# Optimization experiments

Hardware: AMD Instinct MI355X
Metric: run time of the kernel (lower is better)

Reference implementation:

```python
import jax, jax.numpy as jnp
import numpy as np

N_NODES = 50000
N_EDGES = 800000
ATOM_DIM = 128
BOND_DIM = 16
HID = 128
STEPS = 4


def setup_inputs() -> dict:
    key = jax.random.key(0)
    k1, k2, k3, k4, k5, k6 = jax.random.split(key, 6)
    atoms = jax.random.normal(k1, (N_NODES, ATOM_DIM), dtype=jnp.float32)
    bonds = jax.random.normal(k2, (N_NODES, BOND_DIM), dtype=jnp.float32)
    pairs = jax.random.randint(k3, (N_EDGES, 2), 0, N_NODES)
    # sort rows by target id (tf.math.segment_sum expects sorted segment ids)
    order = jnp.argsort(pairs[:, 0])
    pairs = pairs[order].astype(jnp.int64)
    # learned parameters (glorot-ish scaling)
    kernel = jax.random.normal(k4, (ATOM_DIM, BOND_DIM * BOND_DIM), dtype=jnp.float32) * (2.0 / (ATOM_DIM + BOND_DIM * BOND_DIM)) ** 0.5
    bias = jnp.zeros((BOND_DIM * BOND_DIM,), dtype=jnp.float32)
    weight_node = jax.random.normal(k5, (BOND_DIM, HID), dtype=jnp.float32) * (2.0 / (BOND_DIM + HID)) ** 0.5
    weight_node_inp = jax.random.normal(k6, (BOND_DIM, HID), dtype=jnp.float32) * (2.0 / (BOND_DIM + HID)) ** 0.5
    return {"atoms": atoms, "bonds": bonds, "pairs": pairs,
            "kernel": kernel, "bias": bias,
            "weight_node": weight_node, "weight_node_inp": weight_node_inp}


def reference(atoms, bonds, pairs, kernel, bias, weight_node, weight_node_inp):
    n, bd = bonds.shape
    # per-node transform -> [N, bd, bd] message matrices
    A = (atoms @ kernel + bias).reshape(n, bd, bd)
    src = pairs[:, 0]
    nbr = pairs[:, 1]
    # gather bonds of neighbors, apply source-node matrix per edge: [E, bd]
    trans = jnp.einsum('eij,ej->ei', A[src], bonds[nbr])
    # scatter-add back to nodes keyed on pairs[:,0]
    aggregate = jax.ops.segment_sum(trans, src, num_segments=n)  # [N, bd]
    # step loop: aggregate is never updated in the original, so each step
    # computes the identical result; compute once and replicate.
    nodes = aggregate @ weight_node            # [N, hid]
    edges = jax.nn.relu(bonds @ weight_node_inp)  # [N, hid]
    result = jax.nn.relu(nodes + edges)
    return jnp.stack([result] * STEPS)  # [steps, N, hid]
```

## Files before the change

### kernel.cpp

```cpp
#include <hip/hip_runtime.h>

typedef __attribute__((ext_vector_type(8))) short bf16x8;
typedef __attribute__((ext_vector_type(4))) float f32x4;

constexpr int N       = 50000;
constexpr int NE      = 800000;
constexpr int AD      = 128;
constexpr int BD      = 16;
constexpr int BD2     = 256;
constexpr int HIDDEN  = 128;
constexpr int NB      = 64;
constexpr int SSTR    = 20;
constexpr int OSTR    = 132;

__device__ inline short f2bf(float f) {
    union U { float f; unsigned u; } v; v.f = f;
    unsigned r = v.u + 0x7fffu + ((v.u >> 16) & 1u);
    return (short)(r >> 16);
}

__global__ __launch_bounds__(256) void prep_frags(
    const float* __restrict__ kmat,
    const float* __restrict__ Wn,
    const float* __restrict__ Wi,
    short* __restrict__ kbf,
    short* __restrict__ wbf)
{
    int t = blockIdx.x * 256 + threadIdx.x;
    if (t < 4096) {
        int u = t >> 6, l = t & 63;
        int nf = u >> 2, kk = u & 3;
        int col = nf * 16 + (l & 15);
        int k0  = kk * 32 + (l >> 4) * 8;
        bf16x8 o;
#pragma unroll
        for (int j = 0; j < 8; ++j) o[j] = f2bf(kmat[(size_t)(k0 + j) * BD2 + col]);
        *(bf16x8*)(kbf + (size_t)t * 8) = o;
    } else if (t < 4096 + 1024) {
        int t2 = t - 4096;
        int u = t2 >> 6, l = t2 & 63;
        int m = u >> 3, nf2 = u & 7;
        const float* W = m ? Wi : Wn;
        int col = nf2 * 16 + (l & 15);
        int k0  = (l >> 4) * 8;
        bf16x8 o;
#pragma unroll
        for (int j = 0; j < 8; ++j) {
            int k = k0 + j;
            o[j] = (k < 16) ? f2bf(W[(size_t)k * HIDDEN + col]) : (short)0;
        }
        *(bf16x8*)(wbf + (size_t)t2 * 8) = o;
    }
}

__global__ __launch_bounds__(256) void scatter_tile(
    const int*  __restrict__ pairs,
    const float* __restrict__ bonds,
    float* __restrict__ S)
{
    __shared__ float st[NB * SSTR];

    const int tid = threadIdx.x;
    const int nb  = blockIdx.x * NB;

    for (int i = tid; i < NB * SSTR; i += 256) st[i] = 0.f;

    int wlo = nb * 16 - 4096; if (wlo < 0) wlo = 0;
    int whi = (nb + NB) * 16 + 4096; if (whi > NE) whi = NE;
    if (wlo > 0  && pairs[2 * wlo] >= nb)      wlo = 0;
    if (whi < NE && pairs[2 * whi] <  nb + NB) whi = NE;
    int eLo, eHi;
    {
        int s = wlo, e = whi;
        while (s < e) { int m = (s + e) >> 1; if (pairs[2 * m] < nb) s = m + 1; else e = m; }
        eLo = s;
    }
    {
        int s = eLo, e = whi;
        while (s < e) { int m = (s + e) >> 1; if (pairs[2 * m] < nb + NB) s = m + 1; else e = m; }
        eHi = s;
    }
    __syncthreads();

    {
        const int g = tid >> 4;
        const int c = tid & 15;
        const int nE = eHi - eLo;
        const int cg = (nE + 15) >> 4;
        int gs = eLo + g * cg;
        int ge = gs + cg; if (ge > eHi) ge = eHi;
        int cur = -1; float acc = 0.f;
        int e = gs;
        for (; e + 4 <= ge; e += 4) {
            int2 pb[4]; float vb[4];
#pragma unroll
            for (int i = 0; i < 4; ++i) pb[i] = *(const int2*)(pairs + 2 * (e + i));
#pragma unroll
            for (int i = 0; i < 4; ++i) vb[i] = bonds[(size_t)pb[i].y * BD + c];
#pragma unroll
            for (int i = 0; i < 4; ++i) {
                if (pb[i].x != cur) {
                    if (cur >= 0) atomicAdd(&st[(cur - nb) * SSTR + c], acc);
                    acc = 0.f; cur = pb[i].x;
                }
                acc += vb[i];
            }
        }
        for (; e < ge; ++e) {
            int2 p = *(const int2*)(pairs + 2 * e);
            float v = bonds[(size_t)p.y * BD + c];
            if (p.x != cur) {
                if (cur >= 0) atomicAdd(&st[(cur - nb) * SSTR + c], acc);
                acc = 0.f; cur = p.x;
            }
            acc += v;
        }
        if (cur >= 0) atomicAdd(&st[(cur - nb) * SSTR + c], acc);
    }
    __syncthreads();

    {
        int node = tid >> 2;
        int c4   = (tid & 3) * 4;
        if (nb + node < N) {
            f32x4 v = *(const f32x4*)(&st[node * SSTR + c4]);
            *(f32x4*)(S + (size_t)(nb + node) * BD + c4) = v;
        }
    }
}

__global__ __launch_bounds__(256, 3) void gemm_contract(
    const float* __restrict__ atoms,
    const short* __restrict__ kbf,
    const float* __restrict__ bias,
    float* Sagg)
{
    __shared__ float ag[NB * SSTR];

    const int tid = threadIdx.x;
    const int w   = tid >> 6;
    const int l   = tid & 63;
    const int lq  = l >> 4;
    const int lj  = l & 15;
    const int nb  = blockIdx.x * NB;

    bf16x8 afrag[4][4];
    float4 sval[4];
#pragma unroll
    for (int ng = 0; ng < 4; ++ng) {
        int arow = nb + ng * 16 + lj; if (arow >= N) arow = N - 1;
        const float* ap = atoms + (size_t)arow * AD + lq * 8;
#pragma unroll
        for (int kk = 0; kk < 4; ++kk) {
            float4 a0 = *(const float4*)(ap + kk * 32);
            float4 a1 = *(const float4*)(ap + kk * 32 + 4);
            bf16x8 af;
            af[0] = f2bf(a0.x); af[1] = f2bf(a0.y); af[2] = f2bf(a0.z); af[3] = f2bf(a0.w);
            af[4] = f2bf(a1.x); af[5] = f2bf(a1.y); af[6] = f2bf(a1.z); af[7] = f2bf(a1.w);
            afrag[ng][kk] = af;
        }
        sval[ng] = *(const float4*)(Sagg + (size_t)arow * BD + lq * 4);
    }

    const bf16x8* kb = (const bf16x8*)kbf;
    float aggf[4][4];
#pragma unroll
    for (int nfl = 0; nfl < 4; ++nfl) {
        const int nf = w * 4 + nfl;
        f32x4 acc[4];
#pragma unroll
        for (int ng = 0; ng < 4; ++ng) acc[ng] = (f32x4){0.f, 0.f, 0.f, 0.f};
#pragma unroll
        for (int kk = 0; kk < 4; ++kk) {
            bf16x8 b = kb[(size_t)(nf * 4 + kk) * 64 + l];
#pragma unroll
            for (int ng = 0; ng < 4; ++ng)
                acc[ng] = __builtin_amdgcn_mfma_f32_16x16x32_bf16(b, afrag[ng][kk], acc[ng], 0, 0, 0);
        }
        float4 bv = *(const float4*)(bias + nf * 16 + lq * 4);
#pragma unroll
        for (int ng = 0; ng < 4; ++ng) {
            float q = (acc[ng][0] + bv.x) * sval[ng].x
                    + (acc[ng][1] + bv.y) * sval[ng].y
                    + (acc[ng][2] + bv.z) * sval[ng].z
                    + (acc[ng][3] + bv.w) * sval[ng].w;
            q += __shfl_xor(q, 16);
            q += __shfl_xor(q, 32);
            aggf[nfl][ng] = q;
        }
    }

#pragma unroll
    for (int ng = 0; ng < 4; ++ng) {
        float v = aggf[0][ng];
        v = (lq == 1) ? aggf[1][ng] : v;
        v = (lq == 2) ? aggf[2][ng] : v;
        v = (lq == 3) ? aggf[3][ng] : v;
        ag[(ng * 16 + lj) * SSTR + w * 4 + lq] = v;
    }
    __syncthreads();

    {
        int node = tid >> 2;
        int c4   = (tid & 3) * 4;
        if (nb + node < N) {
            f32x4 v = *(const f32x4*)(&ag[node * SSTR + c4]);
            *(f32x4*)(Sagg + (size_t)(nb + node) * BD + c4) = v;
        }
    }
}

__global__ __launch_bounds__(256) void epilogue_store(
    const float* __restrict__ agg,
    const float* __restrict__ bonds,
    const short* __restrict__ wbf,
    float* __restrict__ out)
{
    __shared__ float lds[NB * OSTR];

    const int tid = threadIdx.x;
    const int w   = tid >> 6;
    const int l   = tid & 63;
    const int lq  = l >> 4;
    const int lj  = l & 15;
    const int nb  = blockIdx.x * NB;
    const int wrow = nb + w * 16;

    int arow = wrow + lj; if (arow >= N) arow = N - 1;

    bf16x8 agg_a  = (bf16x8){0,0,0,0,0,0,0,0};
    bf16x8 bond_a = (bf16x8){0,0,0,0,0,0,0,0};
    {
        int half = lq & 1;
        float4 g0 = *(const float4*)(agg   + (size_t)arow * BD + half * 8);
        float4 g1 = *(const float4*)(agg   + (size_t)arow * BD + half * 8 + 4);
        float4 b0 = *(const float4*)(bonds + (size_t)arow * BD + half * 8);
        float4 b1 = *(const float4*)(bonds + (size_t)arow * BD + half * 8 + 4);
        if (lq < 2) {
            agg_a[0] = f2bf(g0.x); agg_a[1] = f2bf(g0.y); agg_a[2] = f2bf(g0.z); agg_a[3] = f2bf(g0.w);
            agg_a[4] = f2bf(g1.x); agg_a[5] = f2bf(g1.y); agg_a[6] = f2bf(g1.z); agg_a[7] = f2bf(g1.w);
            bond_a[0] = f2bf(b0.x); bond_a[1] = f2bf(b0.y); bond_a[2] = f2bf(b0.z); bond_a[3] = f2bf(b0.w);
            bond_a[4] = f2bf(b1.x); bond_a[5] = f2bf(b1.y); bond_a[6] = f2bf(b1.z); bond_a[7] = f2bf(b1.w);
        }
    }

    const bf16x8* wb = (const bf16x8*)wbf;
#pragma unroll
    for (int nf2 = 0; nf2 < 8; ++nf2) {
        bf16x8 wn_f = wb[(size_t)nf2 * 64 + l];
        bf16x8 wi_f = wb[(size_t)(8 + nf2) * 64 + l];
        f32x4 e = __builtin_amdgcn_mfma_f32_16x16x32_bf16(
            bond_a, wi_f, (f32x4){0.f, 0.f, 0.f, 0.f}, 0, 0, 0);
        e[0] = fmaxf(e[0], 0.f); e[1] = fmaxf(e[1], 0.f);
        e[2] = fmaxf(e[2], 0.f); e[3] = fmaxf(e[3], 0.f);
        f32x4 o = __builtin_amdgcn_mfma_f32_16x16x32_bf16(agg_a, wn_f, e, 0, 0, 0);
#pragma unroll
        for (int r = 0; r < 4; ++r) {
            int nl = w * 16 + 4 * lq + r;
            lds[nl * OSTR + nf2 * 16 + lj] = fmaxf(o[r], 0.f);
        }
    }
    __syncthreads();

#pragma unroll
    for (int p = 0; p < 8; ++p) {
        int idx  = tid + 256 * p;
        int nl   = idx >> 5;
        int h4   = (idx & 31) * 4;
        int node = nb + nl;
        if (node < N) {
            f32x4 v = *(const f32x4*)(&lds[nl * OSTR + h4]);
            float* dst = out + (size_t)node * HIDDEN + h4;
#pragma unroll
            for (int s = 0; s < 4; ++s) {
                __builtin_nontemporal_store(v, (f32x4*)(dst + (size_t)s * N * HIDDEN));
            }
        }
    }
}

extern "C" void kernel_launch(void* const* d_in, const int* in_sizes, int n_in,
                              void* d_out, int out_size, void* d_ws, size_t ws_size,
                              hipStream_t stream)
{
    const float* atoms = (const float*)d_in[0];
    const float* bonds = (const float*)d_in[1];
    const int*   pairs = (const int*)d_in[2];
    const float* kmat  = (const float*)d_in[3];
    const float* bias  = (const float*)d_in[4];
    const float* Wn    = (const float*)d_in[5];
    const float* Wi    = (const float*)d_in[6];
    float* out = (float*)d_out;

    short* kbf  = (short*)d_ws;
    short* wbf  = kbf + 4096 * 8;
    float* Sagg = (float*)(wbf + 1024 * 8);

    const int nblk = (N + NB - 1) / NB;

    prep_frags<<<20, 256, 0, stream>>>(kmat, Wn, Wi, kbf, wbf);
    scatter_tile<<<nblk, 256, 0, stream>>>(pairs, bonds, Sagg);
    gemm_contract<<<nblk, 256, 0, stream>>>(atoms, kbf, bias, Sagg);
    epilogue_store<<<nblk, 256, 0, stream>>>(Sagg, bonds, wbf, out);
}
```

Before: 76.62 us.

## Shrink scatter/contract node tiles and split epilogue output copies across grid

The scatter and contraction kernels now process 32 nodes per block instead of 64, which creates more blocks. The contraction kernel's occupancy hint is raised to 4 and its weight-fragment loads are hoisted out of the MFMA loop. The epilogue gets a second grid dimension of 4: each block recomputes its tile and writes a single step copy with plain stores, replacing one block writing all four copies with nontemporal stores. This spreads the large output write over more blocks. The cost is recomputing the epilogue four times and losing the nontemporal store hint.

```diff
diff --git a/kernel.cpp b/kernel.cpp
--- a/kernel.cpp
+++ b/kernel.cpp
@@ -9,7 +9,8 @@
 constexpr int BD      = 16;
 constexpr int BD2     = 256;
 constexpr int HIDDEN  = 128;
-constexpr int NB      = 64;
+constexpr int NBS     = 32;
+constexpr int NBE     = 64;
 constexpr int SSTR    = 20;
 constexpr int OSTR    = 132;
 
@@ -58,17 +59,17 @@
     const float* __restrict__ bonds,
     float* __restrict__ S)
 {
-    __shared__ float st[NB * SSTR];
+    __shared__ float st[NBS * SSTR];
 
     const int tid = threadIdx.x;
-    const int nb  = blockIdx.x * NB;
-
-    for (int i = tid; i < NB * SSTR; i += 256) st[i] = 0.f;
+    const int nb  = blockIdx.x * NBS;
+
+    for (int i = tid; i < NBS * SSTR; i += 256) st[i] = 0.f;
 
     int wlo = nb * 16 - 4096; if (wlo < 0) wlo = 0;
-    int whi = (nb + NB) * 16 + 4096; if (whi > NE) whi = NE;
-    if (wlo > 0  && pairs[2 * wlo] >= nb)      wlo = 0;
-    if (whi < NE && pairs[2 * whi] <  nb + NB) whi = NE;
+    int whi = (nb + NBS) * 16 + 4096; if (whi > NE) whi = NE;
+    if (wlo > 0  && pairs[2 * wlo] >= nb)       wlo = 0;
+    if (whi < NE && pairs[2 * whi] <  nb + NBS) whi = NE;
     int eLo, eHi;
     {
         int s = wlo, e = whi;
@@ -77,7 +78,7 @@
     }
     {
         int s = eLo, e = whi;
-        while (s < e) { int m = (s + e) >> 1; if (pairs[2 * m] < nb + NB) s = m + 1; else e = m; }
+        while (s < e) { int m = (s + e) >> 1; if (pairs[2 * m] < nb + NBS) s = m + 1; else e = m; }
         eHi = s;
     }
     __syncthreads();
@@ -119,7 +120,7 @@
     }
     __syncthreads();
 
-    {
+    if (tid < NBS * 4) {
         int node = tid >> 2;
         int c4   = (tid & 3) * 4;
         if (nb + node < N) {
@@ -129,83 +130,88 @@
     }
 }
 
-__global__ __launch_bounds__(256, 3) void gemm_contract(
+__global__ __launch_bounds__(256, 4) void gemm_contract(
     const float* __restrict__ atoms,
     const short* __restrict__ kbf,
     const float* __restrict__ bias,
-    float* Sagg)
-{
-    __shared__ float ag[NB * SSTR];
+    const float* __restrict__ S,
+    float* __restrict__ agg)
+{
+    __shared__ float ag[NBS * SSTR];
 
     const int tid = threadIdx.x;
     const int w   = tid >> 6;
     const int l   = tid & 63;
     const int lq  = l >> 4;
     const int lj  = l & 15;
-    const int nb  = blockIdx.x * NB;
-
-    bf16x8 afrag[4][4];
-    float4 sval[4];
-#pragma unroll
-    for (int ng = 0; ng < 4; ++ng) {
+    const int nb  = blockIdx.x * NBS;
+
+    bf16x8 afrag[2][4];
+    float4 sval[2];
+#pragma unroll
+    for (int ng = 0; ng < 2; ++ng) {
         int arow = nb + ng * 16 + lj; if (arow >= N) arow = N - 1;
         const float* ap = atoms + (size_t)arow * AD + lq * 8;
+        sval[ng] = *(const float4*)(S + (size_t)arow * BD + lq * 4);
 #pragma unroll
         for (int kk = 0; kk < 4; ++kk) {
             float4 a0 = *(const float4*)(ap + kk * 32);
             float4 a1 = *(const float4*)(ap + kk * 32 + 4);
-            bf16x8 af;
-            af[0] = f2bf(a0.x); af[1] = f2bf(a0.y); af[2] = f2bf(a0.z); af[3] = f2bf(a0.w);
-            af[4] = f2bf(a1.x); af[5] = f2bf(a1.y); af[6] = f2bf(a1.z); af[7] = f2bf(a1.w);
-            afrag[ng][kk] = af;
-        }
-        sval[ng] = *(const float4*)(Sagg + (size_t)arow * BD + lq * 4);
+            bf16x8 t;
+            t[0] = f2bf(a0.x); t[1] = f2bf(a0.y); t[2] = f2bf(a0.z); t[3] = f2bf(a0.w);
+            t[4] = f2bf(a1.x); t[5] = f2bf(a1.y); t[6] = f2bf(a1.z); t[7] = f2bf(a1.w);
+            afrag[ng][kk] = t;
+        }
     }
 
     const bf16x8* kb = (const bf16x8*)kbf;
-    float aggf[4][4];
+    float aggf[2][4];
 #pragma unroll
     for (int nfl = 0; nfl < 4; ++nfl) {
         const int nf = w * 4 + nfl;
-        f32x4 acc[4];
-#pragma unroll
-        for (int ng = 0; ng < 4; ++ng) acc[ng] = (f32x4){0.f, 0.f, 0.f, 0.f};
+        bf16x8 b[4];
+#pragma unroll
+        for (int kk = 0; kk < 4; ++kk)
+            b[kk] = kb[(size_t)(nf * 4 + kk) * 64 + l];
+        f32x4 acc[2];
+#pragma unroll
+        for (int ng = 0; ng < 2; ++ng) acc[ng] = (f32x4){0.f, 0.f, 0.f, 0.f};
 #pragma unroll
         for (int kk = 0; kk < 4; ++kk) {
-            bf16x8 b = kb[(size_t)(nf * 4 + kk) * 64 + l];
-#pragma unroll
-            for (int ng = 0; ng < 4; ++ng)
-                acc[ng] = __builtin_amdgcn_mfma_f32_16x16x32_bf16(b, afrag[ng][kk], acc[ng], 0, 0, 0);
+#pragma unroll
+            for (int ng = 0; ng < 2; ++ng)
+                acc[ng] = __builtin_amdgcn_mfma_f32_16x16x32_bf16(
+                    b[kk], afrag[ng][kk], acc[ng], 0, 0, 0);
         }
         float4 bv = *(const float4*)(bias + nf * 16 + lq * 4);
 #pragma unroll
-        for (int ng = 0; ng < 4; ++ng) {
+        for (int ng = 0; ng < 2; ++ng) {
             float q = (acc[ng][0] + bv.x) * sval[ng].x
                     + (acc[ng][1] + bv.y) * sval[ng].y
                     + (acc[ng][2] + bv.z) * sval[ng].z
                     + (acc[ng][3] + bv.w) * sval[ng].w;
             q += __shfl_xor(q, 16);
             q += __shfl_xor(q, 32);
-            aggf[nfl][ng] = q;
-        }
-    }
-
-#pragma unroll
-    for (int ng = 0; ng < 4; ++ng) {
-        float v = aggf[0][ng];
-        v = (lq == 1) ? aggf[1][ng] : v;
-        v = (lq == 2) ? aggf[2][ng] : v;
-        v = (lq == 3) ? aggf[3][ng] : v;
+            aggf[ng][nfl] = q;
+        }
+    }
+
+#pragma unroll
+    for (int ng = 0; ng < 2; ++ng) {
+        float v = aggf[ng][0];
+        v = (lq == 1) ? aggf[ng][1] : v;
+        v = (lq == 2) ? aggf[ng][2] : v;
+        v = (lq == 3) ? aggf[ng][3] : v;
         ag[(ng * 16 + lj) * SSTR + w * 4 + lq] = v;
     }
     __syncthreads();
 
-    {
+    if (tid < NBS * 4) {
         int node = tid >> 2;
         int c4   = (tid & 3) * 4;
         if (nb + node < N) {
             f32x4 v = *(const f32x4*)(&ag[node * SSTR + c4]);
-            *(f32x4*)(Sagg + (size_t)(nb + node) * BD + c4) = v;
+            *(f32x4*)(agg + (size_t)(nb + node) * BD + c4) = v;
         }
     }
 }
@@ -216,14 +222,15 @@
     const short* __restrict__ wbf,
     float* __restrict__ out)
 {
-    __shared__ float lds[NB * OSTR];
+    __shared__ float lds[NBE * OSTR];
 
     const int tid = threadIdx.x;
     const int w   = tid >> 6;
     const int l   = tid & 63;
     const int lq  = l >> 4;
     const int lj  = l & 15;
-    const int nb  = blockIdx.x * NB;
+    const int nb  = blockIdx.x * NBE;
+    const int cp  = blockIdx.y;
     const int wrow = nb + w * 16;
 
     int arow = wrow + lj; if (arow >= N) arow = N - 1;
@@ -270,11 +277,7 @@
         int node = nb + nl;
         if (node < N) {
             f32x4 v = *(const f32x4*)(&lds[nl * OSTR + h4]);
-            float* dst = out + (size_t)node * HIDDEN + h4;
-#pragma unroll
-            for (int s = 0; s < 4; ++s) {
-                __builtin_nontemporal_store(v, (f32x4*)(dst + (size_t)s * N * HIDDEN));
-            }
+            *(f32x4*)(out + ((size_t)cp * N + node) * HIDDEN + h4) = v;
         }
     }
 }
@@ -296,10 +299,11 @@
     short* wbf  = kbf + 4096 * 8;
     float* Sagg = (float*)(wbf + 1024 * 8);
 
-    const int nblk = (N + NB - 1) / NB;
+    const int nblk32 = (N + NBS - 1) / NBS;
+    const int nblk64 = (N + NBE - 1) / NBE;
 
     prep_frags<<<20, 256, 0, stream>>>(kmat, Wn, Wi, kbf, wbf);
-    scatter_tile<<<nblk, 256, 0, stream>>>(pairs, bonds, Sagg);
-    gemm_contract<<<nblk, 256, 0, stream>>>(atoms, kbf, bias, Sagg);
-    epilogue_store<<<nblk, 256, 0, stream>>>(Sagg, bonds, wbf, out);
-}
+    scatter_tile<<<nblk32, 256, 0, stream>>>(pairs, bonds, Sagg);
+    gemm_contract<<<nblk32, 256, 0, stream>>>(atoms, kbf, bias, Sagg, Sagg);
+    epilogue_store<<<dim3(nblk64, 4), 256, 0, stream>>>(Sagg, bonds, wbf, out);
+}
```

Measured after the change: 85.06 us. 1.11x slower.
